# Optimization experiments

Hardware: AMD Instinct MI355X
Metric: run time of the kernel (lower is better)

Reference implementation:

```python
import math
import jax, jax.numpy as jnp
import numpy as np

H = 64; W = 64; SX = 2; SY = 2; RATIO = 0.5; HEADS = 8


def _tome_indices(metric):
    # no_rand variant of bipartite_soft_matching_random2d: dst token is the
    # top-left element of every (SY, SX) block; indices computed under stop_gradient
    # (torch.no_grad in the original).
    m = jax.lax.stop_gradient(metric)
    B, N, _ = m.shape
    hsy, wsx = H // SY, W // SX
    num_dst = hsy * wsx
    dst_mask = ((jnp.arange(H)[:, None] % SY == 0) & (jnp.arange(W)[None, :] % SX == 0)).reshape(-1)
    order = jnp.argsort(jnp.where(dst_mask, -1, 0), stable=True)  # -1 entries (dst) first
    b_idx, a_idx = order[:num_dst], order[num_dst:]               # [num_dst], [N-num_dst]
    mn = m / jnp.linalg.norm(m, axis=-1, keepdims=True)
    a, b = mn[:, a_idx], mn[:, b_idx]
    scores = jnp.einsum('bsc,bdc->bsd', a, b)                      # [B, Ns, Nd] cosine sims
    r = min(a.shape[1], int(N * RATIO))
    node_max = scores.max(-1)
    node_idx = scores.argmax(-1)
    edge_idx = jnp.argsort(-node_max, axis=-1, stable=True)        # descending
    unm_idx, src_idx = edge_idx[:, r:], edge_idx[:, :r]
    dst_idx = jnp.take_along_axis(node_idx, src_idx, axis=1)
    return a_idx, b_idx, unm_idx, src_idx, dst_idx


def _merge(x, idxs):
    a_idx, b_idx, unm_idx, src_idx, dst_idx = idxs
    src, dst = x[:, a_idx], x[:, b_idx]
    unm = jnp.take_along_axis(src, unm_idx[..., None], axis=1)
    s = jnp.take_along_axis(src, src_idx[..., None], axis=1)
    bg = jnp.broadcast_to(jnp.arange(x.shape[0])[:, None], dst_idx.shape)
    sums = jnp.zeros_like(dst).at[bg, dst_idx].add(s)
    counts = jnp.zeros(dst.shape[:2], x.dtype).at[bg, dst_idx].add(1.0)
    dst = (dst + sums) / (1.0 + counts[..., None])  # scatter_reduce 'mean', include_self
    return jnp.concatenate([unm, dst], axis=1)


def _unmerge(x, idxs, N):
    a_idx, b_idx, unm_idx, src_idx, dst_idx = idxs
    unm_len = unm_idx.shape[1]
    unm, dst = x[:, :unm_len], x[:, unm_len:]
    s = jnp.take_along_axis(dst, dst_idx[..., None], axis=1)
    B, _, c = x.shape
    out = jnp.zeros((B, N, c), x.dtype)
    out = out.at[:, b_idx].set(dst)
    bgu = jnp.broadcast_to(jnp.arange(B)[:, None], unm_idx.shape)
    out = out.at[bgu, a_idx[unm_idx]].set(unm)
    bgs = jnp.broadcast_to(jnp.arange(B)[:, None], src_idx.shape)
    out = out.at[bgs, a_idx[src_idx]].set(s)
    return out


def _ln(x, g, b):
    mu = x.mean(-1, keepdims=True)
    var = ((x - mu) ** 2).mean(-1, keepdims=True)
    return (x - mu) / jnp.sqrt(var + 1e-5) * g + b


def _attn(x, ctx, wq, wk, wv, wo, bo):
    B, Nq, C = x.shape
    dh = C // HEADS
    q = (x @ wq).reshape(B, Nq, HEADS, dh)
    k = (ctx @ wk).reshape(B, -1, HEADS, dh)
    v = (ctx @ wv).reshape(B, -1, HEADS, dh)
    s = jnp.einsum('bqhd,bkhd->bhqk', q, k) * (1.0 / math.sqrt(dh))
    p = jax.nn.softmax(s, axis=-1)
    o = jnp.einsum('bhqk,bkhd->bqhd', p, v).reshape(B, Nq, C)
    return o @ wo + bo


def _forward(net, context, ln1_g, ln1_b, ln2_g, ln2_b, ln3_g, ln3_b,
             attn1_wq, attn1_wk, attn1_wv, attn1_wo, attn1_bo,
             attn2_wq, attn2_wk, attn2_wv, attn2_wo, attn2_bo,
             ff_w1, ff_b1, ff_w2, ff_b2):
    N = net.shape[1]
    idxs = _tome_indices(net)
    # self-attn with ToMe merge/unmerge (merge_attn=True)
    xm = _merge(_ln(net, ln1_g, ln1_b), idxs)
    net = _unmerge(_attn(xm, xm, attn1_wq, attn1_wk, attn1_wv, attn1_wo, attn1_bo), idxs, N) + net
    # cross-attn (merge_crossattn=False)
    net = _attn(_ln(net, ln2_g, ln2_b), context, attn2_wq, attn2_wk, attn2_wv, attn2_wo, attn2_bo) + net
    # GEGLU feed-forward (merge_mlp=False)
    h1 = _ln(net, ln3_g, ln3_b) @ ff_w1 + ff_b1
    xh, gh = jnp.split(h1, 2, axis=-1)
    net = (xh * jax.nn.gelu(gh, approximate=False)) @ ff_w2 + ff_b2 + net
    return net


def setup_inputs() -> dict:
    key = jax.random.key(0)
    ks = jax.random.split(key, 12)
    B, N, C, Lc, Dc = 2, 4096, 320, 77, 768
    dff = 4 * C
    w = lambda k, s: jax.random.normal(k, s, jnp.float32) * 0.02
    return {
        'net': jax.random.normal(ks[0], (B, N, C), jnp.float32),
        'context': jax.random.normal(ks[1], (B, Lc, Dc), jnp.float32),
        'ln1_g': jnp.ones((C,), jnp.float32), 'ln1_b': jnp.zeros((C,), jnp.float32),
        'ln2_g': jnp.ones((C,), jnp.float32), 'ln2_b': jnp.zeros((C,), jnp.float32),
        'ln3_g': jnp.ones((C,), jnp.float32), 'ln3_b': jnp.zeros((C,), jnp.float32),
        'attn1_wq': w(ks[2], (C, C)), 'attn1_wk': w(ks[3], (C, C)),
        'attn1_wv': w(ks[4], (C, C)), 'attn1_wo': w(ks[5], (C, C)),
        'attn1_bo': jnp.zeros((C,), jnp.float32),
        'attn2_wq': w(ks[6], (C, C)), 'attn2_wk': w(ks[7], (Dc, C)),
        'attn2_wv': w(ks[8], (Dc, C)), 'attn2_wo': w(ks[9], (C, C)),
        'attn2_bo': jnp.zeros((C,), jnp.float32),
        'ff_w1': w(ks[10], (C, 2 * dff)), 'ff_b1': jnp.zeros((2 * dff,), jnp.float32),
        'ff_w2': w(ks[11], (dff, C)), 'ff_b2': jnp.zeros((C,), jnp.float32),
    }


def reference(net, context, ln1_g, ln1_b, ln2_g, ln2_b, ln3_g, ln3_b,
              attn1_wq, attn1_wk, attn1_wv, attn1_wo, attn1_bo,
              attn2_wq, attn2_wk, attn2_wv, attn2_wo, attn2_bo,
              ff_w1, ff_b1, ff_w2, ff_b2):
    return _forward(net, context, ln1_g, ln1_b, ln2_g, ln2_b, ln3_g, ln3_b,
                    attn1_wq, attn1_wk, attn1_wv, attn1_wo, attn1_bo,
                    attn2_wq, attn2_wk, attn2_wv, attn2_wo, attn2_bo,
                    ff_w1, ff_b1, ff_w2, ff_b2)
```

## Files before the change

### kernel.cpp

```cpp
#include <hip/hip_runtime.h>

typedef __attribute__((ext_vector_type(8))) short bf16x8;
typedef __attribute__((ext_vector_type(4))) float f32x4;

constexpr int kB   = 2;
constexpr int kN   = 4096;
constexpr int kC   = 320;
constexpr int kNA  = 3072;
constexpr int kNB  = 1024;
constexpr int kNM  = 2048;
constexpr int kR   = 2048;
constexpr int kH   = 8;
constexpr int kDH  = 40;
constexpr int kLC  = 77;
constexpr int kDC  = 768;
constexpr int kDFF = 1280;

__device__ __forceinline__ unsigned short f2b(float f){
  unsigned u = __float_as_uint(f);
  u += 0x7FFF + ((u>>16)&1);
  return (unsigned short)(u>>16);
}
__device__ __forceinline__ float b2f(unsigned short h){ return __uint_as_float(((unsigned)h)<<16); }

__device__ __forceinline__ float wave_sum(float v){
  #pragma unroll
  for (int m=32;m>=1;m>>=1) v += __shfl_xor(v, m, 64);
  return v;
}
__device__ __forceinline__ int d_arank(int h, int w){
  int base = 32*((h+1)>>1) + 64*(h>>1);
  return base + ((h&1) ? w : (w>>1));
}

constexpr size_t rndB(size_t x){ return (x + 255) & ~(size_t)255; }
constexpr size_t B_mnA  = 0;
constexpr size_t B_mnB  = rndB(B_mnA + (size_t)kB*kNA*kC*4);
constexpr size_t B_y32  = rndB(B_mnB + (size_t)kB*kNB*kC*4);
constexpr size_t B_xm   = rndB(B_y32 + (size_t)kB*kN*kC*4);
constexpr size_t B_xo1  = rndB(B_xm  + (size_t)kB*kNM*kC*4);
constexpr size_t B_net1 = rndB(B_xo1 + (size_t)kB*kNM*kC*4);
constexpr size_t B_H    = 0;
constexpr size_t B_net2 = rndB(B_net1 + (size_t)kB*kN*kC*4);
constexpr size_t B_G    = rndB(B_net2 + (size_t)kB*kN*kC*4);
constexpr size_t B_QKb  = rndB(B_G    + (size_t)kB*kN*kDFF*2);
constexpr size_t B_Vtg  = rndB(B_QKb  + (size_t)kB*kNM*640*2);
constexpr size_t B_yb   = rndB(B_Vtg  + (size_t)320*kB*kNM*2);
constexpr size_t B_xmb  = rndB(B_yb   + (size_t)kB*kN*kC*2);
constexpr size_t B_Ao1b = rndB(B_xmb  + (size_t)kB*kNM*kC*2);
constexpr size_t B_Q2b  = rndB(B_Ao1b + (size_t)kB*kNM*kC*2);
constexpr size_t B_Ao2b = rndB(B_Q2b  + (size_t)kB*kN*kC*2);
constexpr size_t B_KV2b = rndB(B_Ao2b + (size_t)kB*kN*kC*2);
constexpr size_t B_Vt2g = rndB(B_KV2b + (size_t)kB*kLC*640*2);
constexpr size_t B_ctxb = rndB(B_Vt2g + (size_t)kB*320*80*2);
constexpr size_t B_Wqkv = rndB(B_ctxb + (size_t)kB*kLC*kDC*2);
constexpr size_t B_Wo1  = rndB(B_Wqkv + (size_t)960*320*2);
constexpr size_t B_Wq2  = rndB(B_Wo1  + (size_t)320*320*2);
constexpr size_t B_Wkv2 = rndB(B_Wq2  + (size_t)320*320*2);
constexpr size_t B_Wo2  = rndB(B_Wkv2 + (size_t)640*768*2);
constexpr size_t B_Wff1 = rndB(B_Wo2  + (size_t)320*320*2);
constexpr size_t B_Wff2 = rndB(B_Wff1 + (size_t)2560*320*2);
constexpr size_t B_cnt  = rndB(B_Wff2 + (size_t)320*1280*2);
constexpr size_t B_pack = rndB(B_cnt  + (size_t)kB*kNB*4);
constexpr size_t B_rank = rndB(B_pack + (size_t)kB*kNA*8);
constexpr size_t B_nidx = rndB(B_rank + (size_t)kB*kNA*4);
constexpr size_t B_mrg  = rndB(B_nidx + (size_t)kB*kNA*4);
constexpr size_t B_slot = rndB(B_mrg  + (size_t)kB*kNA*4);
constexpr size_t B_unml = rndB(B_slot + (size_t)kB*kNA*4);
constexpr size_t B_ucnt = rndB(B_unml + (size_t)kB*kNB*4);
constexpr size_t B_aidx = rndB(B_ucnt + 64);

__global__ void k_gather(const float* __restrict__ net, float* __restrict__ mA, float* __restrict__ mB,
                         unsigned long long* __restrict__ pack, int* __restrict__ ucnt,
                         int* __restrict__ a_idx, int* __restrict__ rank){
  int blk = blockIdx.x; int b = blk >> 12; int t = blk & 4095;
  int lane = threadIdx.x;
  int gid = blk*64 + lane;
  if (gid < kB*kNA){ pack[gid] = 0ull; rank[gid] = 0; }
  if (gid < kB) ucnt[gid] = 0;
  if (gid < kN){
    int h = gid>>6, w = gid&63;
    if ((h|w)&1) a_idx[d_arank(h,w)] = gid;
  }
  const float* xp = net + ((size_t)b*kN + t)*kC;
  float v[5]; float s2 = 0.f;
  #pragma unroll
  for (int i=0;i<5;i++){ float f = xp[lane + i*64]; v[i]=f; s2 += f*f; }
  s2 = wave_sum(s2);
  float rn = 1.0f / sqrtf(s2);
  int h=t>>6, w=t&63;
  float* dp;
  if (!((h|w)&1)) dp = mB + ((size_t)b*kNB + ((h>>1)*32+(w>>1)))*kC;
  else            dp = mA + ((size_t)b*kNA + d_arank(h,w))*kC;
  #pragma unroll
  for (int i=0;i<5;i++) dp[lane + i*64] = v[i]*rn;
}

__global__ __launch_bounds__(256) void k_scores(const float* __restrict__ mA, const float* __restrict__ mB,
                                                unsigned long long* __restrict__ pack){
  __shared__ __align__(16) float As[16][68];
  __shared__ __align__(16) float Bs[16][68];
  const int b = blockIdx.z;
  const int m0 = blockIdx.x*64, n0 = blockIdx.y*64;
  const int tid = threadIdx.x;
  const int mr = tid>>4, nc = tid&15;
  const int lr = tid>>2, lc4 = (tid&3)*4;
  const float* Ab = mA + (size_t)b*kNA*kC;
  const float* Bb = mB + (size_t)b*kNB*kC;
  float acc[4][4] = {};
  for (int k0=0; k0<kC; k0+=16){
    __syncthreads();
    {
      float4 av = *reinterpret_cast<const float4*>(&Ab[(size_t)(m0+lr)*kC + k0 + lc4]);
      As[lc4+0][lr]=av.x; As[lc4+1][lr]=av.y; As[lc4+2][lr]=av.z; As[lc4+3][lr]=av.w;
      float4 bv = *reinterpret_cast<const float4*>(&Bb[(size_t)(n0+lr)*kC + k0 + lc4]);
      Bs[lc4+0][lr]=bv.x; Bs[lc4+1][lr]=bv.y; Bs[lc4+2][lr]=bv.z; Bs[lc4+3][lr]=bv.w;
    }
    __syncthreads();
    #pragma unroll
    for (int kk=0;kk<16;kk++){
      const float4 a4 = *reinterpret_cast<const float4*>(&As[kk][mr*4]);
      const float4 b4 = *reinterpret_cast<const float4*>(&Bs[kk][nc*4]);
      const float aa[4]={a4.x,a4.y,a4.z,a4.w};
      const float bb[4]={b4.x,b4.y,b4.z,b4.w};
      #pragma unroll
      for (int i=0;i<4;i++)
        #pragma unroll
        for (int j=0;j<4;j++)
          acc[i][j] = fmaf(aa[i], bb[j], acc[i][j]);
    }
  }
  #pragma unroll
  for (int i=0;i<4;i++){
    float bs = acc[i][0]; int bj = n0 + nc*4;
    #pragma unroll
    for (int j=1;j<4;j++){
      float v = acc[i][j];
      if (v > bs){ bs=v; bj=n0+nc*4+j; }
    }
    #pragma unroll
    for (int off=1; off<16; off<<=1){
      float os = __shfl_xor(bs, off, 16);
      int   oj = __shfl_xor(bj, off, 16);
      if (os > bs || (os == bs && oj < bj)){ bs=os; bj=oj; }
    }
    if (nc == 0){
      unsigned int u = __float_as_uint(bs);
      unsigned int key = (u & 0x80000000u) ? ~u : (u | 0x80000000u);
      unsigned long long pk = ((unsigned long long)key << 32) |
                              (unsigned long long)(0xFFFFFFFFu - (unsigned int)bj);
      atomicMax(&pack[(size_t)b*kNA + m0 + mr*4 + i], pk);
    }
  }
}
__global__ __launch_bounds__(256) void k_rank_part(const unsigned long long* __restrict__ pack,
                                                   int* __restrict__ rank){
  __shared__ unsigned int keys[256];
  const int b = blockIdx.z;
  const int i = blockIdx.x*256 + threadIdx.x;
  const int j0 = blockIdx.y*256;
  const unsigned long long* pb = pack + (size_t)b*kNA;
  keys[threadIdx.x] = (unsigned int)(pb[j0 + threadIdx.x]>>32);
  unsigned int ki = (unsigned int)(pb[i]>>32);
  __syncthreads();
  int cnt = 0;
  #pragma unroll 8
  for (int jj=0;jj<256;jj++){
    unsigned int kj = keys[jj];
    int j = j0 + jj;
    cnt += (kj > ki) || (kj == ki && j < i);
  }
  atomicAdd(&rank[(size_t)b*kNA + i], cnt);
}
__global__ void k_rank_assign(const unsigned long long* __restrict__ pack, const int* __restrict__ rank,
                              int* __restrict__ node_idx, int* __restrict__ merged,
                              int* __restrict__ slot_of, int* __restrict__ unm_list,
                              int* __restrict__ ucnt){
  int b = blockIdx.y;
  int i = blockIdx.x*256 + threadIdx.x;
  unsigned long long p = pack[(size_t)b*kNA + i];
  node_idx[(size_t)b*kNA + i] = (int)(0xFFFFFFFFu - (unsigned int)(p & 0xFFFFFFFFull));
  int mg = rank[(size_t)b*kNA + i] < kR;
  merged[(size_t)b*kNA + i] = mg;
  if (!mg){
    int s = atomicAdd(&ucnt[b], 1);
    unm_list[(size_t)b*kNB + s] = i;
    slot_of[(size_t)b*kNA + i] = s;
  }
}

template<bool OB>
__global__ void k_ln(const float* __restrict__ x, const float* __restrict__ g,
                     const float* __restrict__ be, void* __restrict__ yv){
  const int row = blockIdx.x;
  const int lane = threadIdx.x;
  const float* xp = x + (size_t)row*kC;
  float v[5]; float s=0.f, s2=0.f;
  #pragma unroll
  for (int i=0;i<5;i++){ float f = xp[lane + i*64]; v[i]=f; s+=f; s2+=f*f; }
  s = wave_sum(s); s2 = wave_sum(s2);
  float mu = s * (1.0f/kC);
  float var = s2 * (1.0f/kC) - mu*mu;
  float rstd = rsqrtf(var + 1e-5f);
  #pragma unroll
  for (int i=0;i<5;i++){
    int c = lane + i*64;
    float o = (v[i]-mu)*rstd*g[c] + be[c];
    if (OB) ((unsigned short*)yv)[(size_t)row*kC + c] = f2b(o);
    else    ((float*)yv)[(size_t)row*kC + c] = o;
  }
}

__global__ void k_merge_ud(const float* __restrict__ y, const int* __restrict__ a_idx,
                           const int* __restrict__ unm_list, unsigned short* __restrict__ xmb,
                           float* __restrict__ xm, float* __restrict__ cnt){
  int blk = blockIdx.x;
  int lane = threadIdx.x;
  if (blk < kB*kNB){
    int b = blk >> 10; int s = blk & 1023;
    int i = unm_list[(size_t)b*kNB + s];
    int t = a_idx[i];
    const float* sp = y + ((size_t)b*kN + t)*kC;
    unsigned short* dp = xmb + ((size_t)b*kNM + s)*kC;
    #pragma unroll
    for (int q=0;q<5;q++) dp[lane+q*64] = f2b(sp[lane+q*64]);
  } else {
    blk -= kB*kNB;
    int b = blk >> 10; int j = blk & 1023;
    int t = 128*(j>>5) + 2*(j&31);
    const float* sp = y + ((size_t)b*kN + t)*kC;
    float* dp = xm + ((size_t)b*kNM + kNB + j)*kC;
    #pragma unroll
    for (int q=0;q<5;q++) dp[lane+q*64] = sp[lane+q*64];
    if (lane==0) cnt[(size_t)b*kNB + j] = 1.0f;
  }
}
__global__ void k_merge_src(const float* __restrict__ y, const int* __restrict__ a_idx,
                            const int* __restrict__ merged, const int* __restrict__ node_idx,
                            float* __restrict__ xm, float* __restrict__ cnt){
  int blk = blockIdx.x; int b = blk / kNA; int i = blk % kNA;
  if (!merged[(size_t)b*kNA + i]) return;
  int t = a_idx[i]; int j = node_idx[(size_t)b*kNA + i];
  const float* sp = y + ((size_t)b*kN + t)*kC;
  float* dp = xm + ((size_t)b*kNM + kNB + j)*kC;
  int lane = threadIdx.x;
  #pragma unroll
  for (int q=0;q<5;q++) atomicAdd(&dp[lane+q*64], sp[lane+q*64]);
  if (lane==0) atomicAdd(&cnt[(size_t)b*kNB + j], 1.0f);
}
__global__ void k_merge_scale(const float* __restrict__ xm, const float* __restrict__ cnt,
                              unsigned short* __restrict__ xmb){
  int blk = blockIdx.x; int b = blk >> 10; int j = blk & 1023;
  float inv = 1.0f / cnt[(size_t)b*kNB + j];
  const float* sp = xm + ((size_t)b*kNM + kNB + j)*kC;
  unsigned short* dp = xmb + ((size_t)b*kNM + kNB + j)*kC;
  int lane = threadIdx.x;
  #pragma unroll
  for (int q=0;q<5;q++) dp[lane+q*64] = f2b(sp[lane+q*64]*inv);
}

__global__ __launch_bounds__(256) void k_wt_all(
    const float* __restrict__ w0, const float* __restrict__ w1, const float* __restrict__ w2,
    const float* __restrict__ w3, const float* __restrict__ w4, const float* __restrict__ w5,
    const float* __restrict__ w6, const float* __restrict__ w7, const float* __restrict__ w8,
    const float* __restrict__ w9,
    unsigned short* __restrict__ Wqkv, unsigned short* __restrict__ Wo1,
    unsigned short* __restrict__ Wq2,  unsigned short* __restrict__ Wkv2,
    unsigned short* __restrict__ Wo2,  unsigned short* __restrict__ Wff1,
    unsigned short* __restrict__ Wff2,
    const float* __restrict__ ctx, unsigned short* __restrict__ ctxb,
    unsigned short* __restrict__ Vt2){
  const int bid = blockIdx.x;
  const int tid = threadIdx.x;
  if (bid >= 570){
    int base = (bid-570)*2048 + tid*8;
    #pragma unroll
    for (int j=0;j<8;j++){
      int i = base + j;
      if (i < kB*kLC*kDC) ctxb[i] = f2b(ctx[i]);
    }
    if (bid == 570){
      for (int r=tid; r<kB*320; r+=256){
        Vt2[(size_t)r*80 + 77] = 0; Vt2[(size_t)r*80 + 78] = 0; Vt2[(size_t)r*80 + 79] = 0;
      }
    }
    return;
  }
  const int jb[11]   = {0,25,50,75,100,125,185,245,270,470,570};
  const float* srcs[10] = {w0,w1,w2,w3,w4,w5,w6,w7,w8,w9};
  unsigned short* dsts[10] = {Wqkv, Wqkv+320*320, Wqkv+640*320, Wo1, Wq2,
                              Wkv2, Wkv2+320*768, Wo2, Wff1, Wff2};
  const int Kd[10] = {320,320,320,320,320,768,768,320,320,1280};
  const int Nd[10] = {320,320,320,320,320,320,320,320,2560,320};
  int job = 0;
  while (bid >= jb[job+1]) job++;
  int local = bid - jb[job];
  const int Nt = (Nd[job]+63)>>6;
  int k0 = (local / Nt)*64, n0 = (local % Nt)*64;
  const float* W = srcs[job];
  unsigned short* Wt = dsts[job];
  const int K = Kd[job], N = Nd[job];
  __shared__ float tile[64][65];
  #pragma unroll
  for (int l=0;l<16;l++){
    int e = tid + l*256; int r = e>>6, c = e&63;
    int gk = k0+r, gn = n0+c;
    tile[r][c] = (gk<K && gn<N) ? W[(size_t)gk*N+gn] : 0.f;
  }
  __syncthreads();
  #pragma unroll
  for (int l=0;l<16;l++){
    int e = tid + l*256; int r = e>>6, c = e&63;
    int gn = n0+r, gk = k0+c;
    if (gn<N && gk<K) Wt[(size_t)gn*K+gk] = f2b(tile[c][r]);
  }
}

template<typename OT, bool BIAS, bool RES, int SVM>
__global__ __launch_bounds__(256) void k_bgemm(const unsigned short* __restrict__ A,
    const unsigned short* __restrict__ Bt, const float* __restrict__ bias,
    const float* __restrict__ resid, OT* __restrict__ out, unsigned short* __restrict__ vt,
    int M, int N, int K, int ldo){
  constexpr int LDK = 72;
  __shared__ unsigned short As[128*LDK];
  __shared__ unsigned short Bs[128*LDK];
  const int tid = threadIdx.x;
  const int m0 = blockIdx.x*128, n0 = blockIdx.y*128;
  const int wid = tid>>6, lane = tid&63;
  const int wm = (wid>>1)*64, wn = (wid&1)*64;
  const int lr = lane&15, quad = lane>>4;
  const f32x4 zero4 = {0.f,0.f,0.f,0.f};
  f32x4 acc[4][4];
  #pragma unroll
  for (int i=0;i<4;i++)
    #pragma unroll
    for (int j=0;j<4;j++) acc[i][j] = zero4;
  for (int k0=0; k0<K; k0+=64){
    __syncthreads();
    #pragma unroll
    for (int l=0;l<4;l++){
      int e = tid + l*256;
      int row = e>>3, seg = (e&7)*8;
      int gm = m0+row;
      uint4 va = (gm<M) ? *reinterpret_cast<const uint4*>(&A[(size_t)gm*K + k0 + seg])
                        : make_uint4(0u,0u,0u,0u);
      *reinterpret_cast<uint4*>(&As[row*LDK + seg]) = va;
      int gn = n0+row;
      uint4 vb = (gn<N) ? *reinterpret_cast<const uint4*>(&Bt[(size_t)gn*K + k0 + seg])
                        : make_uint4(0u,0u,0u,0u);
      *reinterpret_cast<uint4*>(&Bs[row*LDK + seg]) = vb;
    }
    __syncthreads();
    #pragma unroll
    for (int kk=0; kk<64; kk+=32){
      bf16x8 af[4], bfr[4];
      #pragma unroll
      for (int i=0;i<4;i++) af[i]  = *reinterpret_cast<const bf16x8*>(&As[(wm+i*16+lr)*LDK + kk + quad*8]);
      #pragma unroll
      for (int j=0;j<4;j++) bfr[j] = *reinterpret_cast<const bf16x8*>(&Bs[(wn+j*16+lr)*LDK + kk + quad*8]);
      #pragma unroll
      for (int i=0;i<4;i++)
        #pragma unroll
        for (int j=0;j<4;j++)
          acc[i][j] = __builtin_amdgcn_mfma_f32_16x16x32_bf16(af[i], bfr[j], acc[i][j], 0, 0, 0);
    }
  }
  #pragma unroll
  for (int i=0;i<4;i++){
    #pragma unroll
    for (int j=0;j<4;j++){
      int gn = n0 + wn + j*16 + lr;
      if (gn >= N) continue;
      float bv = BIAS ? bias[gn] : 0.f;
      #pragma unroll
      for (int r=0;r<4;r++){
        int gm = m0 + wm + i*16 + quad*4 + r;
        if (gm >= M) continue;
        float v = acc[i][j][r] + bv;
        if (RES) v += resid[(size_t)gm*ldo + gn];
        if (SVM == 1 && gn >= 640){
          vt[(size_t)(gn-640)*4096 + gm] = f2b(v);
        } else if (SVM == 2 && gn >= 320){
          int bb = gm / 77, tok = gm - bb*77;
          vt[((size_t)bb*320 + (gn-320))*80 + tok] = f2b(v);
        } else {
          if constexpr (sizeof(OT)==2) out[(size_t)gm*ldo + gn] = (OT)f2b(v);
          else                         out[(size_t)gm*ldo + gn] = (OT)v;
        }
      }
    }
  }
}

template<typename OT, bool BIAS, bool RES, int SVM>
__global__ __launch_bounds__(256) void k_bgemm64(const unsigned short* __restrict__ A,
    const unsigned short* __restrict__ Bt, const float* __restrict__ bias,
    const float* __restrict__ resid, OT* __restrict__ out, unsigned short* __restrict__ vt,
    int M, int N, int K, int ldo){
  constexpr int LDK = 72;
  __shared__ unsigned short As[64*LDK];
  __shared__ unsigned short Bs[64*LDK];
  const int tid = threadIdx.x;
  const int m0 = blockIdx.x*64, n0 = blockIdx.y*64;
  const int wid = tid>>6, lane = tid&63;
  const int wm = (wid>>1)*32, wn = (wid&1)*32;
  const int lr = lane&15, quad = lane>>4;
  const f32x4 zero4 = {0.f,0.f,0.f,0.f};
  f32x4 acc[2][2];
  #pragma unroll
  for (int i=0;i<2;i++)
    #pragma unroll
    for (int j=0;j<2;j++) acc[i][j] = zero4;
  for (int k0=0; k0<K; k0+=64){
    __syncthreads();
    #pragma unroll
    for (int l=0;l<2;l++){
      int e = tid + l*256;
      int row = e>>3, seg = (e&7)*8;
      int gm = m0+row;
      uint4 va = (gm<M) ? *reinterpret_cast<const uint4*>(&A[(size_t)gm*K + k0 + seg])
                        : make_uint4(0u,0u,0u,0u);
      *reinterpret_cast<uint4*>(&As[row*LDK + seg]) = va;
      int gn = n0+row;
      uint4 vb = (gn<N) ? *reinterpret_cast<const uint4*>(&Bt[(size_t)gn*K + k0 + seg])
                        : make_uint4(0u,0u,0u,0u);
      *reinterpret_cast<uint4*>(&Bs[row*LDK + seg]) = vb;
    }
    __syncthreads();
    #pragma unroll
    for (int kk=0; kk<64; kk+=32){
      bf16x8 af[2], bfr[2];
      #pragma unroll
      for (int i=0;i<2;i++) af[i]  = *reinterpret_cast<const bf16x8*>(&As[(wm+i*16+lr)*LDK + kk + quad*8]);
      #pragma unroll
      for (int j=0;j<2;j++) bfr[j] = *reinterpret_cast<const bf16x8*>(&Bs[(wn+j*16+lr)*LDK + kk + quad*8]);
      #pragma unroll
      for (int i=0;i<2;i++)
        #pragma unroll
        for (int j=0;j<2;j++)
          acc[i][j] = __builtin_amdgcn_mfma_f32_16x16x32_bf16(af[i], bfr[j], acc[i][j], 0, 0, 0);
    }
  }
  #pragma unroll
  for (int i=0;i<2;i++){
    #pragma unroll
    for (int j=0;j<2;j++){
      int gn = n0 + wn + j*16 + lr;
      if (gn >= N) continue;
      float bv = BIAS ? bias[gn] : 0.f;
      #pragma unroll
      for (int r=0;r<4;r++){
        int gm = m0 + wm + i*16 + quad*4 + r;
        if (gm >= M) continue;
        float v = acc[i][j][r] + bv;
        if (RES) v += resid[(size_t)gm*ldo + gn];
        if (SVM == 1 && gn >= 640){
          vt[(size_t)(gn-640)*4096 + gm] = f2b(v);
        } else if (SVM == 2 && gn >= 320){
          int bb = gm / 77, tok = gm - bb*77;
          vt[((size_t)bb*320 + (gn-320))*80 + tok] = f2b(v);
        } else {
          if constexpr (sizeof(OT)==2) out[(size_t)gm*ldo + gn] = (OT)f2b(v);
          else                         out[(size_t)gm*ldo + gn] = (OT)v;
        }
      }
    }
  }
}

__global__ void k_geglu(const unsigned short* __restrict__ H, unsigned short* __restrict__ G){
  int e = blockIdx.x*256 + threadIdx.x;
  int m = e/160, t = e - m*160;
  const unsigned short* hp = H + (size_t)m*2560 + t*8;
  uint4 xv = *reinterpret_cast<const uint4*>(hp);
  uint4 gv = *reinterpret_cast<const uint4*>(hp + 1280);
  const unsigned short* xu = reinterpret_cast<const unsigned short*>(&xv);
  const unsigned short* gu = reinterpret_cast<const unsigned short*>(&gv);
  unsigned short ov[8];
  #pragma unroll
  for (int d=0; d<8; d++){
    float x = b2f(xu[d]);
    float g = b2f(gu[d]);
    float ge = 0.5f*g*(1.0f + erff(g*0.70710678118654752f));
    ov[d] = f2b(x*ge);
  }
  *reinterpret_cast<uint4*>(G + (size_t)m*1280 + t*8) = *reinterpret_cast<const uint4*>(ov);
}

__global__ __launch_bounds__(256) void k_attn1(const unsigned short* __restrict__ QK,
                                               const unsigned short* __restrict__ Vtg,
                                               unsigned short* __restrict__ Oa){
  constexpr int LP = 72, LV = 136;
  __shared__ unsigned short Qs[64*LP];
  __shared__ unsigned short Ks[128*LP];
  __shared__ unsigned short Vt[48*LV];
  __shared__ unsigned short Ps[64*LV];
  const int b = blockIdx.z, hh = blockIdx.y;
  const int q0 = blockIdx.x*64;
  const int tid = threadIdx.x;
  const int wid = tid>>6, lane = tid&63;
  const int lr = lane&15, quad = lane>>4;
  const int wm = wid*16;
  const float scale = 0.15811388300841898f;
  const unsigned short* Qb = QK + ((size_t)b*kNM + q0)*640 + hh*kDH;
  const unsigned short* Kb = QK + ((size_t)b*kNM)*640 + 320 + hh*kDH;
  const unsigned short* Vb = Vtg + (size_t)hh*kDH*4096 + (size_t)b*kNM;
  const uint4 z4 = make_uint4(0u,0u,0u,0u);
  for (int e=tid; e<192; e+=256){
    int row=e/3, seg=40+(e%3)*8;
    *reinterpret_cast<uint4*>(&Qs[row*LP+seg]) = z4;
  }
  for (int e=tid; e<384; e+=256){
    int row=e/3, seg=40+(e%3)*8;
    *reinterpret_cast<uint4*>(&Ks[row*LP+seg]) = z4;
  }
  for (int e=tid; e<136; e+=256){
    int row=40+e/17, seg=(e%17)*8;
    *reinterpret_cast<uint4*>(&Vt[row*LV+seg]) = z4;
  }
  for (int e=tid; e<320; e+=256){
    int row=e/5, seg=(e%5)*8;
    *reinterpret_cast<uint4*>(&Qs[row*LP+seg]) =
      *reinterpret_cast<const uint4*>(Qb + (size_t)row*640 + seg);
  }
  const f32x4 zf = {0.f,0.f,0.f,0.f};
  f32x4 oacc[3] = {zf, zf, zf};
  float l_i[4] = {0.f, 0.f, 0.f, 0.f};
  for (int kt=0; kt<kNM; kt+=128){
    __syncthreads();
    for (int e=tid; e<640; e+=256){
      int row=e/5, seg=(e%5)*8;
      *reinterpret_cast<uint4*>(&Ks[row*LP+seg]) =
        *reinterpret_cast<const uint4*>(Kb + (size_t)(kt+row)*640 + seg);
    }
    for (int e=tid; e<640; e+=256){
      int d=e>>4, seg=(e&15)*8;
      *reinterpret_cast<uint4*>(&Vt[d*LV+seg]) =
        *reinterpret_cast<const uint4*>(Vb + (size_t)d*4096 + kt + seg);
    }
    __syncthreads();
    f32x4 sacc[8];
    bf16x8 aq0 = *reinterpret_cast<const bf16x8*>(&Qs[(wm+lr)*LP + quad*8]);
    bf16x8 aq1 = *reinterpret_cast<const bf16x8*>(&Qs[(wm+lr)*LP + 32 + quad*8]);
    #pragma unroll
    for (int j=0;j<8;j++){
      bf16x8 bk0 = *reinterpret_cast<const bf16x8*>(&Ks[(j*16+lr)*LP + quad*8]);
      sacc[j] = __builtin_amdgcn_mfma_f32_16x16x32_bf16(aq0, bk0, zf, 0,0,0);
      bf16x8 bk1 = *reinterpret_cast<const bf16x8*>(&Ks[(j*16+lr)*LP + 32 + quad*8]);
      sacc[j] = __builtin_amdgcn_mfma_f32_16x16x32_bf16(aq1, bk1, sacc[j], 0,0,0);
    }
    #pragma unroll
    for (int r=0;r<4;r++){
      int row = wm + quad*4 + r;
      float psum = 0.f;
      #pragma unroll
      for (int j=0;j<8;j++){
        float p = __expf(sacc[j][r]*scale);
        psum += p;
        Ps[row*LV + j*16 + lr] = f2b(p);
      }
      #pragma unroll
      for (int off=1; off<16; off<<=1) psum += __shfl_xor(psum, off, 64);
      l_i[r] += psum;
    }
    #pragma unroll
    for (int s=0;s<4;s++){
      bf16x8 ap = *reinterpret_cast<const bf16x8*>(&Ps[(wm+lr)*LV + s*32 + quad*8]);
      #pragma unroll
      for (int nt=0;nt<3;nt++){
        bf16x8 bv = *reinterpret_cast<const bf16x8*>(&Vt[(nt*16+lr)*LV + s*32 + quad*8]);
        oacc[nt] = __builtin_amdgcn_mfma_f32_16x16x32_bf16(ap, bv, oacc[nt], 0,0,0);
      }
    }
  }
  #pragma unroll
  for (int r=0;r<4;r++){
    float inv = 1.0f / l_i[r];
    unsigned short* Ob = Oa + ((size_t)b*kNM + q0 + wm + quad*4 + r)*kC + hh*kDH;
    #pragma unroll
    for (int nt=0;nt<3;nt++){
      int d = nt*16 + lr;
      if (d < kDH) Ob[d] = f2b(oacc[nt][r]*inv);
    }
  }
}

__global__ __launch_bounds__(256) void k_attn2m(const unsigned short* __restrict__ Q,
                                                const unsigned short* __restrict__ KV,
                                                const unsigned short* __restrict__ Vt2,
                                                unsigned short* __restrict__ Oa){
  constexpr int LP = 72, LP2 = 104;
  __shared__ unsigned short Qs[64*LP];
  __shared__ unsigned short Ks[80*LP];
  __shared__ unsigned short Vts[48*LP2];
  __shared__ unsigned short Ps[64*LP2];
  const int b = blockIdx.z, hh = blockIdx.y;
  const int q0 = blockIdx.x*64;
  const int tid = threadIdx.x;
  const int wid = tid>>6, lane = tid&63;
  const int lr = lane&15, quad = lane>>4;
  const int wm = wid*16;
  const float scale = 0.15811388300841898f;
  const uint4 z4 = make_uint4(0u,0u,0u,0u);
  for (int e=tid; e<576; e+=256) *reinterpret_cast<uint4*>(&Qs[e*8]) = z4;
  for (int e=tid; e<720; e+=256) *reinterpret_cast<uint4*>(&Ks[e*8]) = z4;
  for (int e=tid; e<624; e+=256) *reinterpret_cast<uint4*>(&Vts[e*8]) = z4;
  for (int e=tid; e<832; e+=256) *reinterpret_cast<uint4*>(&Ps[e*8]) = z4;
  __syncthreads();
  for (int e=tid; e<320; e+=256){
    int row=e/5, seg=(e%5)*8;
    *reinterpret_cast<uint4*>(&Qs[row*LP+seg]) =
      *reinterpret_cast<const uint4*>(Q + ((size_t)b*kN + q0 + row)*kC + hh*kDH + seg);
  }
  for (int e=tid; e<385; e+=256){
    int row=e/5, seg=(e%5)*8;
    *reinterpret_cast<uint4*>(&Ks[row*LP+seg]) =
      *reinterpret_cast<const uint4*>(KV + ((size_t)b*kLC + row)*640 + hh*kDH + seg);
  }
  for (int e=tid; e<400; e+=256){
    int d=e/10, seg=(e%10)*8;
    *reinterpret_cast<uint4*>(&Vts[d*LP2+seg]) =
      *reinterpret_cast<const uint4*>(Vt2 + ((size_t)b*320 + hh*kDH + d)*80 + seg);
  }
  __syncthreads();
  const f32x4 zf = {0.f,0.f,0.f,0.f};
  f32x4 sacc[5] = {zf, zf, zf, zf, zf};
  bf16x8 aq0 = *reinterpret_cast<const bf16x8*>(&Qs[(wm+lr)*LP + quad*8]);
  bf16x8 aq1 = *reinterpret_cast<const bf16x8*>(&Qs[(wm+lr)*LP + 32 + quad*8]);
  #pragma unroll
  for (int j=0;j<5;j++){
    bf16x8 bk0 = *reinterpret_cast<const bf16x8*>(&Ks[(j*16+lr)*LP + quad*8]);
    sacc[j] = __builtin_amdgcn_mfma_f32_16x16x32_bf16(aq0, bk0, sacc[j], 0,0,0);
    bf16x8 bk1 = *reinterpret_cast<const bf16x8*>(&Ks[(j*16+lr)*LP + 32 + quad*8]);
    sacc[j] = __builtin_amdgcn_mfma_f32_16x16x32_bf16(aq1, bk1, sacc[j], 0,0,0);
  }
  float l_i[4];
  #pragma unroll
  for (int r=0;r<4;r++){
    float vv[5];
    float rm = -1e30f;
    #pragma unroll
    for (int j=0;j<5;j++){
      int c = j*16 + lr;
      vv[j] = sacc[j][r]*scale;
      if (c < kLC) rm = fmaxf(rm, vv[j]);
    }
    #pragma unroll
    for (int off=1; off<16; off<<=1) rm = fmaxf(rm, __shfl_xor(rm, off, 64));
    float psum = 0.f;
    int row = wm + quad*4 + r;
    #pragma unroll
    for (int j=0;j<5;j++){
      int c = j*16 + lr;
      float p = (c < kLC) ? __expf(vv[j]-rm) : 0.f;
      psum += p;
      Ps[row*LP2 + c] = f2b(p);
    }
    #pragma unroll
    for (int off=1; off<16; off<<=1) psum += __shfl_xor(psum, off, 64);
    l_i[r] = psum;
  }
  f32x4 oacc[3] = {zf, zf, zf};
  #pragma unroll
  for (int s=0;s<3;s++){
    bf16x8 ap = *reinterpret_cast<const bf16x8*>(&Ps[(wm+lr)*LP2 + s*32 + quad*8]);
    #pragma unroll
    for (int nt=0;nt<3;nt++){
      bf16x8 bv = *reinterpret_cast<const bf16x8*>(&Vts[(nt*16+lr)*LP2 + s*32 + quad*8]);
      oacc[nt] = __builtin_amdgcn_mfma_f32_16x16x32_bf16(ap, bv, oacc[nt], 0,0,0);
    }
  }
  #pragma unroll
  for (int r=0;r<4;r++){
    float inv = 1.0f / l_i[r];
    unsigned short* Ob = Oa + ((size_t)b*kN + q0 + wm + quad*4 + r)*kC + hh*kDH;
    #pragma unroll
    for (int nt=0;nt<3;nt++){
      int d = nt*16 + lr;
      if (d < kDH) Ob[d] = f2b(oacc[nt][r]*inv);
    }
  }
}

__global__ void k_unmerge(const float* __restrict__ net, const float* __restrict__ Xo,
                          const int* __restrict__ merged, const int* __restrict__ node_idx,
                          const int* __restrict__ slot_of, float* __restrict__ net1){
  int blk = blockIdx.x; int b = blk >> 12; int t = blk & 4095;
  int h = t>>6, w = t&63;
  int row;
  if (!((h|w)&1)) row = kNB + ((h>>1)*32 + (w>>1));
  else {
    int i = d_arank(h,w);
    row = merged[(size_t)b*kNA+i] ? (kNB + node_idx[(size_t)b*kNA+i]) : slot_of[(size_t)b*kNA+i];
  }
  const float* np_ = net + ((size_t)b*kN + t)*kC;
  const float* xp = Xo + ((size_t)b*kNM + row)*kC;
  float* op = net1 + ((size_t)b*kN + t)*kC;
  int lane = threadIdx.x;
  #pragma unroll
  for (int q=0;q<5;q++){ int c = lane+q*64; op[c] = np_[c] + xp[c]; }
}

extern "C" void kernel_launch(void* const* d_in, const int* in_sizes, int n_in,
                              void* d_out, int out_size, void* d_ws, size_t ws_size,
                              hipStream_t stream){
  const float* net = (const float*)d_in[0];
  const float* ctx = (const float*)d_in[1];
  const float* ln1g=(const float*)d_in[2], *ln1b=(const float*)d_in[3];
  const float* ln2g=(const float*)d_in[4], *ln2b=(const float*)d_in[5];
  const float* ln3g=(const float*)d_in[6], *ln3b=(const float*)d_in[7];
  const float* w1q=(const float*)d_in[8],  *w1k=(const float*)d_in[9];
  const float* w1v=(const float*)d_in[10], *w1o=(const float*)d_in[11];
  const float* b1o=(const float*)d_in[12];
  const float* w2q=(const float*)d_in[13], *w2k=(const float*)d_in[14];
  const float* w2v=(const float*)d_in[15], *w2o=(const float*)d_in[16];
  const float* b2o=(const float*)d_in[17];
  const float* fw1=(const float*)d_in[18], *fb1=(const float*)d_in[19];
  const float* fw2=(const float*)d_in[20], *fb2=(const float*)d_in[21];

  char* ws = (char*)d_ws;
  float* mnA  = (float*)(ws + B_mnA);
  float* mnB  = (float*)(ws + B_mnB);
  float* y32  = (float*)(ws + B_y32);
  float* xm32 = (float*)(ws + B_xm);
  float* Xo1  = (float*)(ws + B_xo1);
  float* net1 = (float*)(ws + B_net1);
  float* net2 = (float*)(ws + B_net2);
  float* cnt  = (float*)(ws + B_cnt);
  unsigned short* Hb   = (unsigned short*)(ws + B_H);
  unsigned short* Gb   = (unsigned short*)(ws + B_G);
  unsigned short* QKb  = (unsigned short*)(ws + B_QKb);
  unsigned short* Vtg  = (unsigned short*)(ws + B_Vtg);
  unsigned short* yb   = (unsigned short*)(ws + B_yb);
  unsigned short* xmb  = (unsigned short*)(ws + B_xmb);
  unsigned short* Ao1b = (unsigned short*)(ws + B_Ao1b);
  unsigned short* Q2b  = (unsigned short*)(ws + B_Q2b);
  unsigned short* Ao2b = (unsigned short*)(ws + B_Ao2b);
  unsigned short* KV2b = (unsigned short*)(ws + B_KV2b);
  unsigned short* Vt2g = (unsigned short*)(ws + B_Vt2g);
  unsigned short* ctxb = (unsigned short*)(ws + B_ctxb);
  unsigned short* Wqkv = (unsigned short*)(ws + B_Wqkv);
  unsigned short* Wo1  = (unsigned short*)(ws + B_Wo1);
  unsigned short* Wq2  = (unsigned short*)(ws + B_Wq2);
  unsigned short* Wkv2 = (unsigned short*)(ws + B_Wkv2);
  unsigned short* Wo2  = (unsigned short*)(ws + B_Wo2);
  unsigned short* Wff1 = (unsigned short*)(ws + B_Wff1);
  unsigned short* Wff2 = (unsigned short*)(ws + B_Wff2);
  unsigned long long* pack = (unsigned long long*)(ws + B_pack);
  int* rnk  = (int*)(ws + B_rank);
  int* nidx = (int*)(ws + B_nidx); int* mrg = (int*)(ws + B_mrg); int* slot = (int*)(ws + B_slot);
  int* unml = (int*)(ws + B_unml); int* ucnt = (int*)(ws + B_ucnt); int* aidx = (int*)(ws + B_aidx);

  k_wt_all<<<628, 256, 0, stream>>>(w1q, w1k, w1v, w1o, w2q, w2k, w2v, w2o, fw1, fw2,
                                    Wqkv, Wo1, Wq2, Wkv2, Wo2, Wff1, Wff2, ctx, ctxb, Vt2g);

  k_gather<<<kB*kN, 64, 0, stream>>>(net, mnA, mnB, pack, ucnt, aidx, rnk);
  k_scores<<<dim3(kNA/64, kNB/64, kB), 256, 0, stream>>>(mnA, mnB, pack);
  k_rank_part  <<<dim3(kNA/256, kNA/256, kB), 256, 0, stream>>>(pack, rnk);
  k_rank_assign<<<dim3(kNA/256, kB), 256, 0, stream>>>(pack, rnk, nidx, mrg, slot, unml, ucnt);
  k_ln<false><<<kB*kN, 64, 0, stream>>>(net, ln1g, ln1b, y32);
  k_merge_ud   <<<kB*kNB*2, 64, 0, stream>>>(y32, aidx, unml, xmb, xm32, cnt);
  k_merge_src  <<<kB*kNA, 64, 0, stream>>>(y32, aidx, mrg, nidx, xm32, cnt);
  k_merge_scale<<<kB*kNB, 64, 0, stream>>>(xm32, cnt, xmb);
  k_bgemm64<unsigned short,false,false,1><<<dim3(64,15), 256, 0, stream>>>(
      xmb, Wqkv, nullptr, nullptr, QKb, Vtg, 4096, 960, 320, 640);
  k_attn1<<<dim3(kNM/64, kH, kB), 256, 0, stream>>>(QKb, Vtg, Ao1b);
  k_bgemm64<float,true,false,0><<<dim3(64,5), 256, 0, stream>>>(
      Ao1b, Wo1, b1o, nullptr, Xo1, nullptr, 4096, 320, 320, 320);
  k_unmerge<<<kB*kN, 64, 0, stream>>>(net, Xo1, mrg, nidx, slot, net1);
  k_ln<true><<<kB*kN, 64, 0, stream>>>(net1, ln2g, ln2b, yb);
  k_bgemm64<unsigned short,false,false,0><<<dim3(128,5), 256, 0, stream>>>(
      yb, Wq2, nullptr, nullptr, Q2b, nullptr, 8192, 320, 320, 320);
  k_bgemm<unsigned short,false,false,2><<<dim3(2,5), 256, 0, stream>>>(
      ctxb, Wkv2, nullptr, nullptr, KV2b, Vt2g, 154, 640, 768, 640);
  k_attn2m<<<dim3(kN/64, kH, kB), 256, 0, stream>>>(Q2b, KV2b, Vt2g, Ao2b);
  k_bgemm64<float,true,true,0><<<dim3(128,5), 256, 0, stream>>>(
      Ao2b, Wo2, b2o, net1, net2, nullptr, 8192, 320, 320, 320);
  k_ln<true><<<kB*kN, 64, 0, stream>>>(net2, ln3g, ln3b, yb);
  k_bgemm<unsigned short,true,false,0><<<dim3(64,20), 256, 0, stream>>>(
      yb, Wff1, fb1, nullptr, Hb, nullptr, 8192, 2560, 320, 2560);
  k_geglu<<<(kB*kN*160+255)/256, 256, 0, stream>>>(Hb, Gb);
  k_bgemm64<float,true,true,0><<<dim3(128,5), 256, 0, stream>>>(
      Gb, Wff2, fb2, net2, (float*)d_out, nullptr, 8192, 320, 1280, 320);
}
```

Measured before the change: 476.7 us.

## Split self-attention keys in two partial passes and enlarge score tile

The first attention kernel now splits its 2048 keys into two halves across separate blocks, doubling the grid. Each block writes unnormalized fp32 partial outputs and row sums, and a new combine kernel adds the halves, normalizes and converts to bf16. Q fragments are loaded straight into registers instead of going through shared memory. The cosine-score GEMM tile grows from 64x64 to 128x64 per block, so each thread computes 8x4 outputs for more reuse. The trade-off is extra global traffic for the fp32 partials, one more launch, and fewer score blocks.

New measurement: 490.9 us. 3.0% more time.

```diff
diff --git a/kernel.cpp b/kernel.cpp
--- a/kernel.cpp
+++ b/kernel.cpp
@@ -69,6 +69,8 @@
 constexpr size_t B_unml = rndB(B_slot + (size_t)kB*kNA*4);
 constexpr size_t B_ucnt = rndB(B_unml + (size_t)kB*kNB*4);
 constexpr size_t B_aidx = rndB(B_ucnt + 64);
+constexpr size_t B_Op   = rndB(B_aidx + (size_t)kNA*4);
+constexpr size_t B_lp   = rndB(B_Op   + (size_t)2*4096*320*4);
 
 __global__ void k_gather(const float* __restrict__ net, float* __restrict__ mA, float* __restrict__ mB,
                          unsigned long long* __restrict__ pack, int* __restrict__ ucnt,
@@ -98,40 +100,44 @@
 
 __global__ __launch_bounds__(256) void k_scores(const float* __restrict__ mA, const float* __restrict__ mB,
                                                 unsigned long long* __restrict__ pack){
-  __shared__ __align__(16) float As[16][68];
+  __shared__ __align__(16) float As[16][136];
   __shared__ __align__(16) float Bs[16][68];
   const int b = blockIdx.z;
-  const int m0 = blockIdx.x*64, n0 = blockIdx.y*64;
+  const int m0 = blockIdx.x*128, n0 = blockIdx.y*64;
   const int tid = threadIdx.x;
   const int mr = tid>>4, nc = tid&15;
-  const int lr = tid>>2, lc4 = (tid&3)*4;
   const float* Ab = mA + (size_t)b*kNA*kC;
   const float* Bb = mB + (size_t)b*kNB*kC;
-  float acc[4][4] = {};
+  float acc[8][4] = {};
+  const int ar = tid>>1, ac8 = (tid&1)*8;
+  const int br = tid>>2, bc4 = (tid&3)*4;
   for (int k0=0; k0<kC; k0+=16){
     __syncthreads();
     {
-      float4 av = *reinterpret_cast<const float4*>(&Ab[(size_t)(m0+lr)*kC + k0 + lc4]);
-      As[lc4+0][lr]=av.x; As[lc4+1][lr]=av.y; As[lc4+2][lr]=av.z; As[lc4+3][lr]=av.w;
-      float4 bv = *reinterpret_cast<const float4*>(&Bb[(size_t)(n0+lr)*kC + k0 + lc4]);
-      Bs[lc4+0][lr]=bv.x; Bs[lc4+1][lr]=bv.y; Bs[lc4+2][lr]=bv.z; Bs[lc4+3][lr]=bv.w;
+      float4 a0 = *reinterpret_cast<const float4*>(&Ab[(size_t)(m0+ar)*kC + k0 + ac8]);
+      float4 a1 = *reinterpret_cast<const float4*>(&Ab[(size_t)(m0+ar)*kC + k0 + ac8 + 4]);
+      As[ac8+0][ar]=a0.x; As[ac8+1][ar]=a0.y; As[ac8+2][ar]=a0.z; As[ac8+3][ar]=a0.w;
+      As[ac8+4][ar]=a1.x; As[ac8+5][ar]=a1.y; As[ac8+6][ar]=a1.z; As[ac8+7][ar]=a1.w;
+      float4 bv = *reinterpret_cast<const float4*>(&Bb[(size_t)(n0+br)*kC + k0 + bc4]);
+      Bs[bc4+0][br]=bv.x; Bs[bc4+1][br]=bv.y; Bs[bc4+2][br]=bv.z; Bs[bc4+3][br]=bv.w;
     }
     __syncthreads();
     #pragma unroll
     for (int kk=0;kk<16;kk++){
-      const float4 a4 = *reinterpret_cast<const float4*>(&As[kk][mr*4]);
-      const float4 b4 = *reinterpret_cast<const float4*>(&Bs[kk][nc*4]);
-      const float aa[4]={a4.x,a4.y,a4.z,a4.w};
+      const float4 a4a = *reinterpret_cast<const float4*>(&As[kk][mr*8]);
+      const float4 a4b = *reinterpret_cast<const float4*>(&As[kk][mr*8+4]);
+      const float4 b4  = *reinterpret_cast<const float4*>(&Bs[kk][nc*4]);
+      const float aa[8]={a4a.x,a4a.y,a4a.z,a4a.w,a4b.x,a4b.y,a4b.z,a4b.w};
       const float bb[4]={b4.x,b4.y,b4.z,b4.w};
       #pragma unroll
-      for (int i=0;i<4;i++)
+      for (int i=0;i<8;i++)
         #pragma unroll
         for (int j=0;j<4;j++)
           acc[i][j] = fmaf(aa[i], bb[j], acc[i][j]);
     }
   }
   #pragma unroll
-  for (int i=0;i<4;i++){
+  for (int i=0;i<8;i++){
     float bs = acc[i][0]; int bj = n0 + nc*4;
     #pragma unroll
     for (int j=1;j<4;j++){
@@ -149,7 +155,7 @@
       unsigned int key = (u & 0x80000000u) ? ~u : (u | 0x80000000u);
       unsigned long long pk = ((unsigned long long)key << 32) |
                               (unsigned long long)(0xFFFFFFFFu - (unsigned int)bj);
-      atomicMax(&pack[(size_t)b*kNA + m0 + mr*4 + i], pk);
+      atomicMax(&pack[(size_t)b*kNA + m0 + mr*8 + i], pk);
     }
   }
 }
@@ -489,27 +495,27 @@
 
 __global__ __launch_bounds__(256) void k_attn1(const unsigned short* __restrict__ QK,
                                                const unsigned short* __restrict__ Vtg,
-                                               unsigned short* __restrict__ Oa){
+                                               float* __restrict__ Opart,
+                                               float* __restrict__ lpart){
   constexpr int LP = 72, LV = 136;
-  __shared__ unsigned short Qs[64*LP];
   __shared__ unsigned short Ks[128*LP];
   __shared__ unsigned short Vt[48*LV];
   __shared__ unsigned short Ps[64*LV];
   const int b = blockIdx.z, hh = blockIdx.y;
-  const int q0 = blockIdx.x*64;
+  const int bx = blockIdx.x;
+  const int q0 = (bx>>1)*64, kz = bx&1;
   const int tid = threadIdx.x;
   const int wid = tid>>6, lane = tid&63;
   const int lr = lane&15, quad = lane>>4;
   const int wm = wid*16;
   const float scale = 0.15811388300841898f;
-  const unsigned short* Qb = QK + ((size_t)b*kNM + q0)*640 + hh*kDH;
   const unsigned short* Kb = QK + ((size_t)b*kNM)*640 + 320 + hh*kDH;
   const unsigned short* Vb = Vtg + (size_t)hh*kDH*4096 + (size_t)b*kNM;
   const uint4 z4 = make_uint4(0u,0u,0u,0u);
-  for (int e=tid; e<192; e+=256){
-    int row=e/3, seg=40+(e%3)*8;
-    *reinterpret_cast<uint4*>(&Qs[row*LP+seg]) = z4;
-  }
+  const unsigned short* Qrow = QK + ((size_t)b*kNM + q0 + wm + lr)*640 + hh*kDH;
+  bf16x8 aq0 = *reinterpret_cast<const bf16x8*>(Qrow + quad*8);
+  bf16x8 aq1 = {0,0,0,0,0,0,0,0};
+  if (quad == 0) aq1 = *reinterpret_cast<const bf16x8*>(Qrow + 32);
   for (int e=tid; e<384; e+=256){
     int row=e/3, seg=40+(e%3)*8;
     *reinterpret_cast<uint4*>(&Ks[row*LP+seg]) = z4;
@@ -518,15 +524,11 @@
     int row=40+e/17, seg=(e%17)*8;
     *reinterpret_cast<uint4*>(&Vt[row*LV+seg]) = z4;
   }
-  for (int e=tid; e<320; e+=256){
-    int row=e/5, seg=(e%5)*8;
-    *reinterpret_cast<uint4*>(&Qs[row*LP+seg]) =
-      *reinterpret_cast<const uint4*>(Qb + (size_t)row*640 + seg);
-  }
   const f32x4 zf = {0.f,0.f,0.f,0.f};
   f32x4 oacc[3] = {zf, zf, zf};
   float l_i[4] = {0.f, 0.f, 0.f, 0.f};
-  for (int kt=0; kt<kNM; kt+=128){
+  const int kbeg = kz*1024, kend = kbeg + 1024;
+  for (int kt=kbeg; kt<kend; kt+=128){
     __syncthreads();
     for (int e=tid; e<640; e+=256){
       int row=e/5, seg=(e%5)*8;
@@ -540,8 +542,6 @@
     }
     __syncthreads();
     f32x4 sacc[8];
-    bf16x8 aq0 = *reinterpret_cast<const bf16x8*>(&Qs[(wm+lr)*LP + quad*8]);
-    bf16x8 aq1 = *reinterpret_cast<const bf16x8*>(&Qs[(wm+lr)*LP + 32 + quad*8]);
     #pragma unroll
     for (int j=0;j<8;j++){
       bf16x8 bk0 = *reinterpret_cast<const bf16x8*>(&Ks[(j*16+lr)*LP + quad*8]);
@@ -573,15 +573,34 @@
       }
     }
   }
+  float* Op = Opart + (size_t)kz*4096*320;
+  float* lp = lpart + (size_t)kz*4096*8;
   #pragma unroll
   for (int r=0;r<4;r++){
-    float inv = 1.0f / l_i[r];
-    unsigned short* Ob = Oa + ((size_t)b*kNM + q0 + wm + quad*4 + r)*kC + hh*kDH;
+    int grow = b*kNM + q0 + wm + quad*4 + r;
     #pragma unroll
     for (int nt=0;nt<3;nt++){
       int d = nt*16 + lr;
-      if (d < kDH) Ob[d] = f2b(oacc[nt][r]*inv);
-    }
+      if (d < kDH) Op[(size_t)grow*320 + hh*kDH + d] = oacc[nt][r];
+    }
+    if (lr == 0) lp[(size_t)grow*8 + hh] = l_i[r];
+  }
+}
+
+__global__ void k_acomb(const float* __restrict__ Opart, const float* __restrict__ lpart,
+                        unsigned short* __restrict__ Ao1b){
+  int row = blockIdx.x;
+  int lane = threadIdx.x;
+  const float* o0 = Opart + (size_t)row*320;
+  const float* o1 = Opart + (size_t)2*4096*320/2 + (size_t)row*320;
+  const float* l0 = lpart + (size_t)row*8;
+  const float* l1 = lpart + (size_t)4096*8 + (size_t)row*8;
+  #pragma unroll
+  for (int i=0;i<5;i++){
+    int c = lane + i*64;
+    int h = c/kDH;
+    float v = (o0[c] + o1[c]) / (l0[h] + l1[h]);
+    Ao1b[(size_t)row*320 + c] = f2b(v);
   }
 }
 
@@ -750,12 +769,14 @@
   int* rnk  = (int*)(ws + B_rank);
   int* nidx = (int*)(ws + B_nidx); int* mrg = (int*)(ws + B_mrg); int* slot = (int*)(ws + B_slot);
   int* unml = (int*)(ws + B_unml); int* ucnt = (int*)(ws + B_ucnt); int* aidx = (int*)(ws + B_aidx);
+  float* Opart = (float*)(ws + B_Op);
+  float* lpart = (float*)(ws + B_lp);
 
   k_wt_all<<<628, 256, 0, stream>>>(w1q, w1k, w1v, w1o, w2q, w2k, w2v, w2o, fw1, fw2,
                                     Wqkv, Wo1, Wq2, Wkv2, Wo2, Wff1, Wff2, ctx, ctxb, Vt2g);
 
   k_gather<<<kB*kN, 64, 0, stream>>>(net, mnA, mnB, pack, ucnt, aidx, rnk);
-  k_scores<<<dim3(kNA/64, kNB/64, kB), 256, 0, stream>>>(mnA, mnB, pack);
+  k_scores<<<dim3(kNA/128, kNB/64, kB), 256, 0, stream>>>(mnA, mnB, pack);
   k_rank_part  <<<dim3(kNA/256, kNA/256, kB), 256, 0, stream>>>(pack, rnk);
   k_rank_assign<<<dim3(kNA/256, kB), 256, 0, stream>>>(pack, rnk, nidx, mrg, slot, unml, ucnt);
   k_ln<false><<<kB*kN, 64, 0, stream>>>(net, ln1g, ln1b, y32);
@@ -764,7 +785,8 @@
   k_merge_scale<<<kB*kNB, 64, 0, stream>>>(xm32, cnt, xmb);
   k_bgemm64<unsigned short,false,false,1><<<dim3(64,15), 256, 0, stream>>>(
       xmb, Wqkv, nullptr, nullptr, QKb, Vtg, 4096, 960, 320, 640);
-  k_attn1<<<dim3(kNM/64, kH, kB), 256, 0, stream>>>(QKb, Vtg, Ao1b);
+  k_attn1<<<dim3((kNM/64)*2, kH, kB), 256, 0, stream>>>(QKb, Vtg, Opart, lpart);
+  k_acomb<<<kB*kNM, 64, 0, stream>>>(Opart, lpart, Ao1b);
   k_bgemm64<float,true,false,0><<<dim3(64,5), 256, 0, stream>>>(
       Ao1b, Wo1, b1o, nullptr, Xo1, nullptr, 4096, 320, 320, 320);
   k_unmerge<<<kB*kN, 64, 0, stream>>>(net, Xo1, mrg, nidx, slot, net1);
```
